# Optimization experiments

Hardware: AMD Instinct MI355X
Metric: run time of the kernel (lower is better)

Reference implementation:

```python
import jax, jax.numpy as jnp
import numpy as np
from jax import lax

DN = ('NCHW', 'OIHW', 'NCHW')


def setup_inputs() -> dict:
    key = jax.random.key(0)
    k1, k2, k3, k4, k5, k6 = jax.random.split(key, 6)
    B, Ch, H, W = 16, 256, 32, 32   # two feature maps of 256 ch -> c = 512
    C = 2 * Ch
    return {
        'x1': jax.random.normal(k1, (B, Ch, H, W), dtype=jnp.float32),
        'x2': jax.random.normal(k2, (B, Ch, H, W), dtype=jnp.float32),
        'g_w': jax.random.normal(k3, (C, C, 3, 3), dtype=jnp.float32) * 0.02,
        'w_w': jax.random.normal(k4, (256, C, 1, 1), dtype=jnp.float32) * 0.05,
        'weight1': jax.random.normal(k5, (C, 16), dtype=jnp.float32) * 0.1,
        'weight2': jax.random.normal(k6, (C, 16), dtype=jnp.float32) * 0.1,
    }


def reference(x1, x2, g_w, w_w, weight1, weight2):
    x = jnp.concatenate([x1, x2], axis=1)            # [b, c, h, w]
    b, c, h, w = x.shape
    g_x = lax.conv_general_dilated(x, g_w, (1, 1), 'SAME', dimension_numbers=DN)
    value = g_x.reshape(b, c, h * w)                 # [b, c, n]
    q = x.reshape(b, c, h * w)                       # query == key source
    sim = jnp.einsum('bcn,bdn->bcd', q, q) * (float(c) ** -0.5)  # [b, c, c]
    random_map = weight1 @ weight2.T                 # [c, c]
    attn = jax.nn.softmax(sim + random_map[None], axis=-1)
    ctx = jnp.einsum('bcd,bdn->bcn', attn, value).reshape(b, c, h, w)
    out = lax.conv_general_dilated(ctx, w_w, (1, 1), 'VALID', dimension_numbers=DN)
    return out
```

## Files before the change

kernel.cpp:

```cpp
#include <hip/hip_runtime.h>
#include <math.h>

typedef float f32x4 __attribute__((ext_vector_type(4)));
typedef short s16x8 __attribute__((ext_vector_type(8)));
typedef unsigned int u32;
typedef unsigned short u16;
typedef u16 u16x4 __attribute__((ext_vector_type(4)));

static constexpr size_t OFF_XT    = 0;
static constexpr size_t OFF_XQ    = 4734976;
static constexpr size_t OFF_ATTNT = 4734976;
static constexpr size_t OFF_WATTN = 6832128;
static constexpr size_t OFF_P0    = 8929280;
static constexpr size_t OFF_P1    = 11026432;
static constexpr size_t OFF_VT    = 8929280;
static constexpr size_t OFF_WA    = 13123584;
static constexpr size_t OFF_RM    = 14303232;
static constexpr size_t OFF_WWB   = 14565376;

__device__ __forceinline__ u16 f2bf(float f) {
    u32 u = __float_as_uint(f);
    u32 r = (u + 0x7FFFu + ((u >> 16) & 1u)) >> 16;
    return (u16)r;
}
__device__ __forceinline__ float bf2f(u16 v) {
    return __uint_as_float(((u32)v) << 16);
}

__device__ __forceinline__ void gload_lds16(const void* g, void* l) {
    __builtin_amdgcn_global_load_lds(
        (const u32 __attribute__((address_space(1)))*)(uintptr_t)g,
        (u32 __attribute__((address_space(3)))*)(uintptr_t)l, 16, 0, 0);
}

__global__ __launch_bounds__(256) void prep_kernel(const float* __restrict__ x1,
                                                   const float* __restrict__ x2,
                                                   const float* __restrict__ gw,
                                                   const float* __restrict__ ww,
                                                   const float* __restrict__ w1,
                                                   const float* __restrict__ w2,
                                                   float* __restrict__ rm,
                                                   u16* __restrict__ wA,
                                                   u16* __restrict__ wwb,
                                                   u16* __restrict__ xT,
                                                   u16* __restrict__ xq) {
    __shared__ __attribute__((aligned(16))) u32 shm[4608];
    const int t = threadIdx.x;
    const int bid = blockIdx.x;

    if (bid < 512) {
        const int co = bid;
        const float* g = gw + (size_t)co * 4608;
        float* lf = (float*)shm;
#pragma unroll
        for (int i = 0; i < 18; ++i) lf[t + i * 256] = g[t + i * 256];
        __syncthreads();
        u16* dst = wA + (size_t)co * 4608;
#pragma unroll
        for (int i = 0; i < 18; ++i) {
            int k = t + i * 256;
            int r = k >> 9, ci = k & 511;
            dst[k] = f2bf(lf[ci * 9 + r]);
        }
    } else if (bid < 2560) {
        int xid = bid - 512;
        int nt = xid & 15;
        int cit = (xid >> 4) & 7;
        int b = xid >> 7;
        int n0 = nt * 64, ci0 = cit * 64;
        const float* src = (ci0 < 256) ? (x1 + ((size_t)(b * 256 + ci0)) * 1024)
                                       : (x2 + ((size_t)(b * 256 + ci0 - 256)) * 1024);
        u16* xqb = xq + ((size_t)(b * 512 + ci0)) * 1024;
        u16* lt = (u16*)shm;
#pragma unroll
        for (int p4 = 0; p4 < 4; ++p4) {
            int ch = (t >> 4) + p4 * 16;
            int px = (t & 15) * 4;
            float4 v = *(const float4*)&src[(size_t)ch * 1024 + n0 + px];
            u16x4 pk = {f2bf(v.x), f2bf(v.y), f2bf(v.z), f2bf(v.w)};
            *(u16x4*)&xqb[(size_t)ch * 1024 + n0 + px] = pk;
            lt[(px + 0) * 65 + ch] = pk[0];
            lt[(px + 1) * 65 + ch] = pk[1];
            lt[(px + 2) * 65 + ch] = pk[2];
            lt[(px + 3) * 65 + ch] = pk[3];
        }
        __syncthreads();
        {
            int px_l = t >> 2, c16 = (t & 3) * 16;
            int n = n0 + px_l;
            int y = n >> 5, x = n & 31;
            int p = (y + 1) * 34 + (x + 1);
            u16* dst = xT + ((size_t)b * 1156 + p) * 512 + ci0 + c16;
            *(s16x8*)&dst[0] = *(const s16x8*)&lt[px_l * 65 + c16];
            *(s16x8*)&dst[8] = *(const s16x8*)&lt[px_l * 65 + c16 + 8];
        }
    } else if (bid < 2576) {
        int b = bid - 2560;
        u16* base = xT + (size_t)b * 1156 * 512;
        s16x8 z = {0, 0, 0, 0, 0, 0, 0, 0};
        for (int idx = t; idx < 132 * 64; idx += 256) {
            int row = idx >> 6, seg = idx & 63;
            int p;
            if (row < 34) p = row;
            else if (row < 68) p = 1122 + (row - 34);
            else if (row < 100) p = (row - 67) * 34;
            else p = (row - 99) * 34 + 33;
            *(s16x8*)&base[(size_t)p * 512 + seg * 8] = z;
        }
    } else if (bid < 3600) {
        int idx = (bid - 2576) * 256 + t;
        int c = idx >> 9, d = idx & 511;
        float s = 0.f;
#pragma unroll
        for (int k = 0; k < 16; ++k) s = fmaf(w1[c * 16 + k], w2[d * 16 + k], s);
        rm[idx] = s;
    } else {
        int idx = (bid - 3600) * 256 + t;
        float4 v = ((const float4*)ww)[idx];
        u16x4 pk = {f2bf(v.x), f2bf(v.y), f2bf(v.z), f2bf(v.w)};
        *(u16x4*)&wwb[(size_t)idx * 4] = pk;
    }
}

__global__ __launch_bounds__(256) void sim_part(const u16* __restrict__ xq,
                                                u16* __restrict__ simP) {
    __shared__ __attribute__((aligned(16))) u16 smem[128 * 128];
    u16* As = smem;
    u16* Bs = smem + 128 * 64;
    const int b = blockIdx.z, m0 = blockIdx.y * 128;
    const int n0 = (blockIdx.x & 3) * 128, khalf = blockIdx.x >> 2;
    const int t = threadIdx.x, w = t >> 6, l = t & 63;
    const u16* xb = xq + (size_t)b * 512 * 1024 + khalf * 512;

    const u16 *agp[4], *bgp[4];
    u16 *ald[4], *bld[4];
#pragma unroll
    for (int i = 0; i < 4; ++i) {
        int rr = w * 8 + i * 32 + (l >> 3);
        int gi = (l & 7) ^ (rr & 7);
        agp[i] = xb + (size_t)(m0 + rr) * 1024 + gi * 8;
        bgp[i] = xb + (size_t)(n0 + rr) * 1024 + gi * 8;
        ald[i] = &As[(w * 8 + i * 32) * 64];
        bld[i] = &Bs[(w * 8 + i * 32) * 64];
    }

    f32x4 acc[4][4] = {};
    const int wm = (w >> 1) * 64, wn = (w & 1) * 64;

    for (int kt = 0; kt < 8; ++kt) {
        int ko = kt << 6;
        if (kt) __syncthreads();
#pragma unroll
        for (int i = 0; i < 4; ++i) gload_lds16(agp[i] + ko, ald[i]);
#pragma unroll
        for (int i = 0; i < 4; ++i) gload_lds16(bgp[i] + ko, bld[i]);
        __syncthreads();
#pragma unroll
        for (int kk = 0; kk < 2; ++kk) {
            int gbase = kk * 4 + (l >> 4);
            s16x8 af[4], bf[4];
#pragma unroll
            for (int i = 0; i < 4; ++i) {
                int row = wm + i * 16 + (l & 15);
                af[i] = *(const s16x8*)&As[row * 64 + ((gbase ^ (row & 7)) << 3)];
            }
#pragma unroll
            for (int j = 0; j < 4; ++j) {
                int row = wn + j * 16 + (l & 15);
                bf[j] = *(const s16x8*)&Bs[row * 64 + ((gbase ^ (row & 7)) << 3)];
            }
#pragma unroll
            for (int i = 0; i < 4; ++i)
#pragma unroll
                for (int j = 0; j < 4; ++j)
                    acc[i][j] = __builtin_amdgcn_mfma_f32_16x16x32_bf16(af[i], bf[j], acc[i][j], 0, 0, 0);
        }
    }

    __syncthreads();
    const int col = l & 15, r4 = (l >> 4) * 4;
#pragma unroll
    for (int i = 0; i < 4; ++i)
#pragma unroll
        for (int j = 0; j < 4; ++j) {
            int n_l = wn + j * 16 + col;
            int m_b = wm + i * 16 + r4;
            u16x4 pk = {f2bf(acc[i][j][0]), f2bf(acc[i][j][1]),
                        f2bf(acc[i][j][2]), f2bf(acc[i][j][3])};
            *(u16x4*)&smem[n_l * 128 + (m_b ^ ((n_l & 15) << 3))] = pk;
        }
    __syncthreads();
    u16* sTb = simP + (size_t)khalf * 4194304 + (size_t)b * 512 * 512;
    {
        int n_l = t >> 1;
#pragma unroll
        for (int rep = 0; rep < 8; ++rep) {
            int c0 = (((t & 1) + rep * 2) << 3);
            s16x8 v = *(const s16x8*)&smem[n_l * 128 + (c0 ^ ((n_l & 15) << 3))];
            *(s16x8*)&sTb[(size_t)(n0 + n_l) * 512 + m0 + c0] = v;
        }
    }
}

__global__ __launch_bounds__(256) void finish_kernel(const u16* __restrict__ p0,
                                                     const u16* __restrict__ p1,
                                                     const float* __restrict__ rm,
                                                     u16* __restrict__ attnT) {
    __shared__ float rml[32 * 513];
    __shared__ float scr[256];
    const int t = threadIdx.x;
    const int b = blockIdx.x >> 4, c0 = (blockIdx.x & 15) * 32;
    const int cl = t & 31, g = t >> 5;
    const float scale = 0.04419417382415922f;

    for (int idx = t; idx < 32 * 512; idx += 256) {
        int c_l = idx >> 9, d = idx & 511;
        rml[c_l * 513 + d] = rm[(size_t)(c0 + c_l) * 512 + d];
    }
    __syncthreads();

    const u16* q0 = p0 + (size_t)b * 262144 + c0 + cl;
    const u16* q1 = p1 + (size_t)b * 262144 + c0 + cl;
    u16* ap = attnT + (size_t)b * 262144 + c0 + cl;
    const float* rp = &rml[cl * 513];

    float s = 0.f;
#pragma unroll 8
    for (int dd = 0; dd < 64; ++dd) {
        int d = g * 64 + dd;
        float v = (bf2f(q0[(size_t)d * 512]) + bf2f(q1[(size_t)d * 512])) * scale + rp[d];
        float e = __expf(v);
        s += e;
        ap[(size_t)d * 512] = f2bf(e);
    }
    scr[t] = s;
    __syncthreads();
    float tot = 0.f;
#pragma unroll
    for (int k = 0; k < 8; ++k) tot += scr[k * 32 + cl];
    float inv = 1.f / tot;
#pragma unroll 8
    for (int dd = 0; dd < 64; ++dd) {
        int d = g * 64 + dd;
        ap[(size_t)d * 512] = f2bf(bf2f(ap[(size_t)d * 512]) * inv);
    }
}

__global__ __launch_bounds__(256) void conv_gemm(const u16* __restrict__ wA,
                                                 const u16* __restrict__ xT,
                                                 u16* __restrict__ vT) {
    __shared__ __attribute__((aligned(16))) u16 smem[128 * 128];
    u16* As = smem;
    u16* Bs = smem + 128 * 64;
    const int b = blockIdx.z, m0 = blockIdx.y * 128, n0 = blockIdx.x * 128;
    const int t = threadIdx.x, w = t >> 6, l = t & 63;
    const u16* xTb = xT + (size_t)b * 1156 * 512;

    int gi[4], pb[4];
    const u16* agp[4];
    u16 *ald[4], *bld[4];
#pragma unroll
    for (int i = 0; i < 4; ++i) {
        int rr = w * 8 + i * 32 + (l >> 3);
        gi[i] = (l & 7) ^ (rr & 7);
        agp[i] = wA + (size_t)(m0 + rr) * 4608 + gi[i] * 8;
        int n = n0 + rr;
        pb[i] = (n >> 5) * 34 + (n & 31);
        ald[i] = &As[(w * 8 + i * 32) * 64];
        bld[i] = &Bs[(w * 8 + i * 32) * 64];
    }

    f32x4 acc[4][4] = {};
    const int wm = (w >> 1) * 64, wn = (w & 1) * 64;

    for (int kt = 0; kt < 72; ++kt) {
        int r = kt >> 3, ci0k = (kt & 7) << 6;
        int rdiv3 = (r * 11) >> 5;
        int poff = rdiv3 * 34 + (r - rdiv3 * 3);
        int aofs = r * 512 + ci0k;
        if (kt) __syncthreads();
#pragma unroll
        for (int i = 0; i < 4; ++i) gload_lds16(agp[i] + aofs, ald[i]);
#pragma unroll
        for (int i = 0; i < 4; ++i)
            gload_lds16(xTb + (size_t)(pb[i] + poff) * 512 + ci0k + gi[i] * 8, bld[i]);
        __syncthreads();

#pragma unroll
        for (int kk = 0; kk < 2; ++kk) {
            int gbase = kk * 4 + (l >> 4);
            s16x8 af[4], bf[4];
#pragma unroll
            for (int i = 0; i < 4; ++i) {
                int row = wm + i * 16 + (l & 15);
                af[i] = *(const s16x8*)&As[row * 64 + ((gbase ^ (row & 7)) << 3)];
            }
#pragma unroll
            for (int j = 0; j < 4; ++j) {
                int row = wn + j * 16 + (l & 15);
                bf[j] = *(const s16x8*)&Bs[row * 64 + ((gbase ^ (row & 7)) << 3)];
            }
#pragma unroll
            for (int i = 0; i < 4; ++i)
#pragma unroll
                for (int j = 0; j < 4; ++j)
                    acc[i][j] = __builtin_amdgcn_mfma_f32_16x16x32_bf16(af[i], bf[j], acc[i][j], 0, 0, 0);
        }
    }

    __syncthreads();
    const int col = l & 15, r4 = (l >> 4) * 4;
#pragma unroll
    for (int i = 0; i < 4; ++i)
#pragma unroll
        for (int j = 0; j < 4; ++j) {
            int n_l = wn + j * 16 + col;
            int co_b = wm + i * 16 + r4;
            u16x4 pk = {f2bf(acc[i][j][0]), f2bf(acc[i][j][1]),
                        f2bf(acc[i][j][2]), f2bf(acc[i][j][3])};
            *(u16x4*)&smem[n_l * 128 + (co_b ^ ((n_l & 15) << 3))] = pk;
        }
    __syncthreads();
    u16* vTb = vT + (size_t)b * 1024 * 512;
    {
        int n_l = t >> 1;
#pragma unroll
        for (int rep = 0; rep < 8; ++rep) {
            int c0 = (((t & 1) + rep * 2) << 3);
            s16x8 v = *(const s16x8*)&smem[n_l * 128 + (c0 ^ ((n_l & 15) << 3))];
            *(s16x8*)&vTb[(size_t)(n0 + n_l) * 512 + m0 + c0] = v;
        }
    }
}

template <int MODE>
__global__ __launch_bounds__(256) void gemm_nt(const u16* __restrict__ A, size_t sA,
                                               const u16* __restrict__ B, size_t sB,
                                               void* __restrict__ Cv, size_t sC,
                                               int K, int ldc) {
    __shared__ __attribute__((aligned(16))) u16 As[128 * 64];
    __shared__ __attribute__((aligned(16))) u16 Bs[128 * 64];
    const int b = blockIdx.z, m0 = blockIdx.y * 128, n0 = blockIdx.x * 128;
    const int t = threadIdx.x, w = t >> 6, l = t & 63;
    const u16* Ab = A + (size_t)b * sA;
    const u16* Bb = B + (size_t)b * sB;

    const u16 *agp[4], *bgp[4];
    u16 *ald[4], *bld[4];
#pragma unroll
    for (int i = 0; i < 4; ++i) {
        int rr = w * 8 + i * 32 + (l >> 3);
        int gi = (l & 7) ^ (rr & 7);
        agp[i] = Ab + (size_t)(m0 + rr) * K + gi * 8;
        bgp[i] = Bb + (size_t)(n0 + rr) * K + gi * 8;
        ald[i] = &As[(w * 8 + i * 32) * 64];
        bld[i] = &Bs[(w * 8 + i * 32) * 64];
    }

    f32x4 acc[4][4] = {};
    const int wm = (w >> 1) * 64, wn = (w & 1) * 64;
    const int nkt = K >> 6;
    for (int kt = 0; kt < nkt; ++kt) {
        int ko = kt << 6;
        if (kt) __syncthreads();
#pragma unroll
        for (int i = 0; i < 4; ++i) gload_lds16(agp[i] + ko, ald[i]);
#pragma unroll
        for (int i = 0; i < 4; ++i) gload_lds16(bgp[i] + ko, bld[i]);
        __syncthreads();
#pragma unroll
        for (int kk = 0; kk < 2; ++kk) {
            int gbase = kk * 4 + (l >> 4);
            s16x8 af[4], bf[4];
#pragma unroll
            for (int i = 0; i < 4; ++i) {
                int row = wm + i * 16 + (l & 15);
                af[i] = *(const s16x8*)&As[row * 64 + ((gbase ^ (row & 7)) << 3)];
            }
#pragma unroll
            for (int j = 0; j < 4; ++j) {
                int row = wn + j * 16 + (l & 15);
                bf[j] = *(const s16x8*)&Bs[row * 64 + ((gbase ^ (row & 7)) << 3)];
            }
#pragma unroll
            for (int i = 0; i < 4; ++i)
#pragma unroll
                for (int j = 0; j < 4; ++j)
                    acc[i][j] = __builtin_amdgcn_mfma_f32_16x16x32_bf16(af[i], bf[j], acc[i][j], 0, 0, 0);
        }
    }

    const int col = l & 15, r4 = (l >> 4) * 4;
#pragma unroll
    for (int i = 0; i < 4; ++i)
#pragma unroll
        for (int j = 0; j < 4; ++j)
#pragma unroll
            for (int reg = 0; reg < 4; ++reg) {
                int m = m0 + wm + i * 16 + r4 + reg;
                int n = n0 + wn + j * 16 + col;
                if (MODE == 1) {
                    u16* C = (u16*)Cv + (size_t)b * sC;
                    C[(size_t)m * ldc + n] = f2bf(acc[i][j][reg]);
                } else {
                    float* C = (float*)Cv + (size_t)b * sC;
                    C[(size_t)m * ldc + n] = acc[i][j][reg];
                }
            }
}

extern "C" void kernel_launch(void* const* d_in, const int* in_sizes, int n_in,
                              void* d_out, int out_size, void* d_ws, size_t ws_size,
                              hipStream_t stream) {
    (void)in_sizes; (void)n_in; (void)out_size; (void)ws_size;
    const float* x1 = (const float*)d_in[0];
    const float* x2 = (const float*)d_in[1];
    const float* gw = (const float*)d_in[2];
    const float* ww = (const float*)d_in[3];
    const float* w1 = (const float*)d_in[4];
    const float* w2 = (const float*)d_in[5];
    float* out = (float*)d_out;
    float* ws = (float*)d_ws;

    u16* xT    = (u16*)(ws + OFF_XT);
    u16* xq    = (u16*)(ws + OFF_XQ);
    u16* attnT = (u16*)(ws + OFF_ATTNT);
    u16* wattn = (u16*)(ws + OFF_WATTN);
    u16* simP  = (u16*)(ws + OFF_P0);
    u16* p0    = (u16*)(ws + OFF_P0);
    u16* p1    = (u16*)(ws + OFF_P1);
    u16* vT    = (u16*)(ws + OFF_VT);
    u16* wA    = (u16*)(ws + OFF_WA);
    float* rm  = ws + OFF_RM;
    u16* wwb   = (u16*)(ws + OFF_WWB);

    prep_kernel<<<3728, 256, 0, stream>>>(x1, x2, gw, ww, w1, w2, rm, wA, wwb, xT, xq);
    sim_part<<<dim3(8, 4, 16), 256, 0, stream>>>(xq, simP);
    finish_kernel<<<256, 256, 0, stream>>>(p0, p1, rm, attnT);
    gemm_nt<1><<<dim3(4, 2, 16), 256, 0, stream>>>(
        wwb, 0, attnT, (size_t)512 * 512, wattn, (size_t)256 * 512, 512, 512);
    conv_gemm<<<dim3(8, 4, 16), 256, 0, stream>>>(wA, xT, vT);
    gemm_nt<2><<<dim3(8, 2, 16), 256, 0, stream>>>(
        wattn, (size_t)256 * 512, vT, (size_t)1024 * 512, out, (size_t)256 * 1024, 512, 1024);
}
```

Baseline: 232.3 us.

## Fold attention and output projection into per-batch effective conv weights

Reassociates the computation: rather than running the 512-out-channel 3x3 conv and then multiplying by the attention-projected matrix, it first forms a per-batch effective weight W_eff = (w_w·attn)·g_w (256×4608) via a transposed copy of the conv weights. It then runs a single 256-out-channel conv directly into the output using split-K with atomic adds. This removes the vT intermediate and the final GEMM and halves the conv's output channels. In exchange it adds a weight transpose, a per-batch weight GEMM, an output memset, fp32 atomics whose summation order is nondeterministic, and processing in two halves of eight batches to bound workspace.

Result: slower. 282.4 us (+21.6%).

```diff
diff --git a/kernel.cpp b/kernel.cpp
--- a/kernel.cpp
+++ b/kernel.cpp
@@ -11,9 +11,10 @@
 static constexpr size_t OFF_XQ    = 4734976;
 static constexpr size_t OFF_ATTNT = 4734976;
 static constexpr size_t OFF_WATTN = 6832128;
+static constexpr size_t OFF_WAT   = 7880704;
 static constexpr size_t OFF_P0    = 8929280;
 static constexpr size_t OFF_P1    = 11026432;
-static constexpr size_t OFF_VT    = 8929280;
+static constexpr size_t OFF_WEFF  = 9060352;
 static constexpr size_t OFF_WA    = 13123584;
 static constexpr size_t OFF_RM    = 14303232;
 static constexpr size_t OFF_WWB   = 14565376;
@@ -246,15 +247,42 @@
     }
 }
 
-__global__ __launch_bounds__(256) void conv_gemm(const u16* __restrict__ wA,
+__global__ __launch_bounds__(256) void transpose_wa(const u16* __restrict__ wA,
+                                                    u16* __restrict__ wAT) {
+    __shared__ u16 lt[64 * 65];
+    const int t = threadIdx.x;
+    const int k0 = blockIdx.x * 64;
+    const int c0 = blockIdx.y * 64;
+    {
+        int co_l = t >> 2, ks = (t & 3) * 16;
+        s16x8 v0 = *(const s16x8*)&wA[(size_t)(c0 + co_l) * 4608 + k0 + ks];
+        s16x8 v1 = *(const s16x8*)&wA[(size_t)(c0 + co_l) * 4608 + k0 + ks + 8];
+#pragma unroll
+        for (int e = 0; e < 8; ++e) {
+            lt[(ks + e) * 65 + co_l] = (u16)v0[e];
+            lt[(ks + 8 + e) * 65 + co_l] = (u16)v1[e];
+        }
+    }
+    __syncthreads();
+    {
+        int k_l = t >> 2, cs = (t & 3) * 16;
+        u16* dst = &wAT[(size_t)(k0 + k_l) * 512 + c0 + cs];
+        *(s16x8*)&dst[0] = *(const s16x8*)&lt[k_l * 65 + cs];
+        *(s16x8*)&dst[8] = *(const s16x8*)&lt[k_l * 65 + cs + 8];
+    }
+}
+
+__global__ __launch_bounds__(256) void conv_weff(const u16* __restrict__ wE,
                                                  const u16* __restrict__ xT,
-                                                 u16* __restrict__ vT) {
+                                                 float* __restrict__ out) {
     __shared__ __attribute__((aligned(16))) u16 smem[128 * 128];
     u16* As = smem;
     u16* Bs = smem + 128 * 64;
-    const int b = blockIdx.z, m0 = blockIdx.y * 128, n0 = blockIdx.x * 128;
+    const int bl = blockIdx.z & 7, kq = blockIdx.z >> 3;
+    const int m0 = blockIdx.y * 128, n0 = blockIdx.x * 128;
     const int t = threadIdx.x, w = t >> 6, l = t & 63;
-    const u16* xTb = xT + (size_t)b * 1156 * 512;
+    const u16* xTb = xT + (size_t)bl * 1156 * 512;
+    const u16* wEb = wE + (size_t)bl * 1179648;
 
     int gi[4], pb[4];
     const u16* agp[4];
@@ -263,7 +291,7 @@
     for (int i = 0; i < 4; ++i) {
         int rr = w * 8 + i * 32 + (l >> 3);
         gi[i] = (l & 7) ^ (rr & 7);
-        agp[i] = wA + (size_t)(m0 + rr) * 4608 + gi[i] * 8;
+        agp[i] = wEb + (size_t)(m0 + rr) * 4608 + gi[i] * 8;
         int n = n0 + rr;
         pb[i] = (n >> 5) * 34 + (n & 31);
         ald[i] = &As[(w * 8 + i * 32) * 64];
@@ -273,12 +301,13 @@
     f32x4 acc[4][4] = {};
     const int wm = (w >> 1) * 64, wn = (w & 1) * 64;
 
-    for (int kt = 0; kt < 72; ++kt) {
+    for (int s = 0; s < 18; ++s) {
+        int kt = kq * 18 + s;
         int r = kt >> 3, ci0k = (kt & 7) << 6;
         int rdiv3 = (r * 11) >> 5;
         int poff = rdiv3 * 34 + (r - rdiv3 * 3);
         int aofs = r * 512 + ci0k;
-        if (kt) __syncthreads();
+        if (s) __syncthreads();
 #pragma unroll
         for (int i = 0; i < 4; ++i) gload_lds16(agp[i] + aofs, ald[i]);
 #pragma unroll
@@ -308,29 +337,18 @@
         }
     }
 
-    __syncthreads();
     const int col = l & 15, r4 = (l >> 4) * 4;
+    float* ob = out + (size_t)bl * 262144;
 #pragma unroll
     for (int i = 0; i < 4; ++i)
 #pragma unroll
         for (int j = 0; j < 4; ++j) {
-            int n_l = wn + j * 16 + col;
-            int co_b = wm + i * 16 + r4;
-            u16x4 pk = {f2bf(acc[i][j][0]), f2bf(acc[i][j][1]),
-                        f2bf(acc[i][j][2]), f2bf(acc[i][j][3])};
-            *(u16x4*)&smem[n_l * 128 + (co_b ^ ((n_l & 15) << 3))] = pk;
-        }
-    __syncthreads();
-    u16* vTb = vT + (size_t)b * 1024 * 512;
-    {
-        int n_l = t >> 1;
-#pragma unroll
-        for (int rep = 0; rep < 8; ++rep) {
-            int c0 = (((t & 1) + rep * 2) << 3);
-            s16x8 v = *(const s16x8*)&smem[n_l * 128 + (c0 ^ ((n_l & 15) << 3))];
-            *(s16x8*)&vTb[(size_t)(n0 + n_l) * 512 + m0 + c0] = v;
-        }
-    }
+            int m = m0 + wm + i * 16 + r4;
+            int n = n0 + wn + j * 16 + col;
+#pragma unroll
+            for (int reg = 0; reg < 4; ++reg)
+                unsafeAtomicAdd(&ob[(size_t)(m + reg) * 1024 + n], acc[i][j][reg]);
+        }
 }
 
 template <int MODE>
@@ -426,20 +444,30 @@
     u16* xq    = (u16*)(ws + OFF_XQ);
     u16* attnT = (u16*)(ws + OFF_ATTNT);
     u16* wattn = (u16*)(ws + OFF_WATTN);
+    u16* wAT   = (u16*)(ws + OFF_WAT);
     u16* simP  = (u16*)(ws + OFF_P0);
     u16* p0    = (u16*)(ws + OFF_P0);
     u16* p1    = (u16*)(ws + OFF_P1);
-    u16* vT    = (u16*)(ws + OFF_VT);
+    u16* weff  = (u16*)(ws + OFF_WEFF);
     u16* wA    = (u16*)(ws + OFF_WA);
     float* rm  = ws + OFF_RM;
     u16* wwb   = (u16*)(ws + OFF_WWB);
 
+    hipMemsetAsync(out, 0, (size_t)16 * 256 * 1024 * 4, stream);
+
     prep_kernel<<<3728, 256, 0, stream>>>(x1, x2, gw, ww, w1, w2, rm, wA, wwb, xT, xq);
     sim_part<<<dim3(8, 4, 16), 256, 0, stream>>>(xq, simP);
     finish_kernel<<<256, 256, 0, stream>>>(p0, p1, rm, attnT);
+    transpose_wa<<<dim3(72, 8), 256, 0, stream>>>(wA, wAT);
     gemm_nt<1><<<dim3(4, 2, 16), 256, 0, stream>>>(
         wwb, 0, attnT, (size_t)512 * 512, wattn, (size_t)256 * 512, 512, 512);
-    conv_gemm<<<dim3(8, 4, 16), 256, 0, stream>>>(wA, xT, vT);
-    gemm_nt<2><<<dim3(8, 2, 16), 256, 0, stream>>>(
-        wattn, (size_t)256 * 512, vT, (size_t)1024 * 512, out, (size_t)256 * 1024, 512, 1024);
-}
+
+    for (int h = 0; h < 2; ++h) {
+        gemm_nt<1><<<dim3(36, 2, 8), 256, 0, stream>>>(
+            wattn + (size_t)h * 8 * 131072, (size_t)131072,
+            wAT, 0,
+            weff, (size_t)256 * 4608, 512, 4608);
+        conv_weff<<<dim3(8, 2, 32), 256, 0, stream>>>(
+            weff, xT + (size_t)h * 8 * 1156 * 512, out + (size_t)h * 8 * 262144);
+    }
+}
```
